# Kernel tuning notes

Measured on AMD Instinct MI355X. Metric: run time of the kernel, lower is better.

Reference implementation:

```python
import jax, jax.numpy as jnp
import numpy as np

S, B, E, H = 2048, 32, 1024, 1024

def setup_inputs() -> dict:
    key = jax.random.key(0)
    k1, k2, k3, k4, k5 = jax.random.split(key, 5)
    h_t = jax.random.normal(k1, (1, B, H), dtype=jnp.float32)
    h_enc = jax.random.normal(k2, (S, B, E), dtype=jnp.float32)
    # nn.Linear weights stored as (out, in); scaled like default init
    W_enc = jax.random.normal(k3, (H, E), dtype=jnp.float32) / np.sqrt(E)
    W_dec = jax.random.normal(k4, (H, H), dtype=jnp.float32) / np.sqrt(H)
    w_score = jax.random.normal(k5, (1, H), dtype=jnp.float32) / np.sqrt(H)
    return {"h_t": h_t, "h_enc": h_enc, "W_enc": W_enc, "W_dec": W_dec, "w_score": w_score}

def reference(h_t, h_enc, W_enc, W_dec, w_score):
    # h_enc: (S,B,E) -> (B,S,E); h_t: (1,B,H) -> (B,1,H)
    he = jnp.transpose(h_enc, (1, 0, 2))
    ht = jnp.transpose(h_t, (1, 0, 2))
    compr_he = jnp.einsum('bse,he->bsh', he, W_enc)          # (B,S,H)
    compr_ht = jnp.einsum('bth,gh->btg', ht, W_dec)          # (B,1,H), broadcasts over S
    # Linear(H,1) -> Tanh -> Softmax over seq dim
    scores = jnp.tanh(jnp.einsum('bsh,oh->bso', compr_he + compr_ht, w_score))  # (B,S,1)
    alphas = jax.nn.softmax(scores, axis=1)                  # (B,S,1)
    context = jnp.sum(he * alphas, axis=1)[None]             # (1,B,E)
    return (context, alphas)
```

## Files before the change

### kernel.cpp

```cpp
#include <hip/hip_runtime.h>
#include <hip/hip_bf16.h>

#define S_DIM 2048
#define B_DIM 32
#define E_DIM 1024
#define H_DIM 1024

#define VCHUNKS 32

#define CH 8
#define WPB 4
#define ROWS_PER_BLOCK (CH * WPB)
#define BLOCKS_PER_B (S_DIM / ROWS_PER_BLOCK)
#define NBLK (B_DIM * BLOCKS_PER_B)


__global__ __launch_bounds__(256) void k1_partial_v(
    const float* __restrict__ W_enc, const float* __restrict__ W_dec,
    const float* __restrict__ w_score, float* __restrict__ penc,
    float* __restrict__ pdec) {
  int bid = blockIdx.x;
  int t = threadIdx.x;
  bool enc = bid < 128;
  int idx = enc ? bid : bid - 128;
  int hc = idx >> 2;
  int e0 = (idx & 3) << 8;
  const float* M = enc ? W_enc : W_dec;
  int h0 = hc * 32;
  float acc = 0.f;
#pragma unroll 8
  for (int r = 0; r < 32; ++r) {
    float w = w_score[h0 + r];
    acc = fmaf(w, M[(size_t)(h0 + r) * E_DIM + e0 + t], acc);
  }
  float* dst = enc ? penc : pdec;
  dst[hc * E_DIM + e0 + t] = acc;
}

__global__ __launch_bounds__(256) void k2_finalize_v(
    const float* __restrict__ penc, const float* __restrict__ pdec,
    float* __restrict__ venc, float* __restrict__ vdec) {
  int g = blockIdx.x * 256 + threadIdx.x;
  bool enc = g < E_DIM;
  const float* p = enc ? penc : pdec;
  int e = enc ? g : g - E_DIM;
  float acc = 0.f;
#pragma unroll 8
  for (int c = 0; c < VCHUNKS; ++c) acc += p[c * E_DIM + e];
  (enc ? venc : vdec)[e] = acc;
}

__device__ __forceinline__ float wave_allreduce_sum(float v) {
#pragma unroll
  for (int off = 1; off < 64; off <<= 1) v += __shfl_xor(v, off, 64);
  return v;
}

__device__ __forceinline__ float fast_tanh(float x) {
  float e2 = __expf(2.f * x);
  return 1.f - 2.f * __builtin_amdgcn_rcpf(e2 + 1.f);
}

__global__ __launch_bounds__(256) void k3_stream(
    const float* __restrict__ h_enc, const float* __restrict__ h_t,
    const float* __restrict__ venc, const float* __restrict__ vdec,
    float* __restrict__ expw, float* __restrict__ pl,
    float* __restrict__ pctx) {
  int bid = blockIdx.x;
  int t = threadIdx.x;
  int w = t >> 6;
  int lane = t & 63;
  int b = bid >> 6;
  int cbi = bid & 63;
  int s0 = cbi * ROWS_PER_BLOCK + w * CH;
  int e_base = lane * 4;

  __shared__ float lctx[WPB][E_DIM];
  __shared__ float ll[WPB];

  float4 ve[4];
#pragma unroll
  for (int k = 0; k < 4; ++k)
    ve[k] = *reinterpret_cast<const float4*>(venc + e_base + k * 256);

  float cb = 0.f;
#pragma unroll
  for (int k = 0; k < 4; ++k) {
    float4 vd = *reinterpret_cast<const float4*>(vdec + e_base + k * 256);
    float4 ht = *reinterpret_cast<const float4*>(h_t + b * H_DIM + e_base + k * 256);
    cb = fmaf(vd.x, ht.x, cb);
    cb = fmaf(vd.y, ht.y, cb);
    cb = fmaf(vd.z, ht.z, cb);
    cb = fmaf(vd.w, ht.w, cb);
  }
  cb = wave_allreduce_sum(cb);

  float4 ctx[4];
#pragma unroll
  for (int k = 0; k < 4; ++k) ctx[k] = make_float4(0.f, 0.f, 0.f, 0.f);
  float lsum = 0.f;

  for (int s = s0; s < s0 + CH; ++s) {
    const float* row = h_enc + ((size_t)s * B_DIM + b) * E_DIM + e_base;
    float4 a[4];
#pragma unroll
    for (int k = 0; k < 4; ++k)
      a[k] = *reinterpret_cast<const float4*>(row + k * 256);

    float d = 0.f;
#pragma unroll
    for (int k = 0; k < 4; ++k) {
      d = fmaf(a[k].x, ve[k].x, d);
      d = fmaf(a[k].y, ve[k].y, d);
      d = fmaf(a[k].z, ve[k].z, d);
      d = fmaf(a[k].w, ve[k].w, d);
    }
    d = wave_allreduce_sum(d);

    float wgt = __expf(fast_tanh(d + cb));
    if (lane == 0) expw[b * S_DIM + s] = wgt;
    lsum += wgt;

#pragma unroll
    for (int k = 0; k < 4; ++k) {
      ctx[k].x = fmaf(wgt, a[k].x, ctx[k].x);
      ctx[k].y = fmaf(wgt, a[k].y, ctx[k].y);
      ctx[k].z = fmaf(wgt, a[k].z, ctx[k].z);
      ctx[k].w = fmaf(wgt, a[k].w, ctx[k].w);
    }
  }

#pragma unroll
  for (int k = 0; k < 4; ++k)
    *reinterpret_cast<float4*>(&lctx[w][e_base + k * 256]) = ctx[k];
  if (lane == 0) ll[w] = lsum;
  __syncthreads();

  {
    int e = t * 4;
    float4 v0 = *reinterpret_cast<const float4*>(&lctx[0][e]);
    float4 v1 = *reinterpret_cast<const float4*>(&lctx[1][e]);
    float4 v2 = *reinterpret_cast<const float4*>(&lctx[2][e]);
    float4 v3 = *reinterpret_cast<const float4*>(&lctx[3][e]);
    float4 r;
    r.x = (v0.x + v1.x) + (v2.x + v3.x);
    r.y = (v0.y + v1.y) + (v2.y + v3.y);
    r.z = (v0.z + v1.z) + (v2.z + v3.z);
    r.w = (v0.w + v1.w) + (v2.w + v3.w);
    *reinterpret_cast<float4*>(pctx + (size_t)bid * E_DIM + e) = r;
    if (t == 0) pl[bid] = (ll[0] + ll[1]) + (ll[2] + ll[3]);
  }
}

__global__ __launch_bounds__(256) void k4_finalize(
    const float* __restrict__ pl, const float* __restrict__ pctx,
    const float* __restrict__ expw, float* __restrict__ out) {
  int bid = blockIdx.x;
  int t = threadIdx.x;
  int lane = t & 63;
  bool isCtx = bid < 256;
  int idx = isCtx ? bid : bid - 256;
  int b = idx >> 3;

  __shared__ float s_l;
  __shared__ float s_half[128];

  if (t < 64) {
    float v = pl[b * BLOCKS_PER_B + lane];
    v = wave_allreduce_sum(v);
    if (lane == 0) s_l = v;
  }
  __syncthreads();
  float lb = s_l;

  if (isCtx) {
    int e0 = (idx & 7) * 128;
    int eo = t & 127;
    int c0 = (t >> 7) * 32;
    const float* base = pctx + (size_t)(b * BLOCKS_PER_B + c0) * E_DIM + e0 + eo;
    float acc = 0.f;
#pragma unroll 8
    for (int c = 0; c < 32; ++c) acc += base[(size_t)c * E_DIM];
    if (t >= 128) s_half[eo] = acc;
    __syncthreads();
    if (t < 128) out[b * E_DIM + e0 + eo] = (acc + s_half[eo]) / lb;
  } else {
    int sb = (idx & 7) * 256;
    int o = b * S_DIM + sb + t;
    out[B_DIM * E_DIM + o] = expw[o] / lb;
  }
}

extern "C" void kernel_launch(void* const* d_in, const int* in_sizes, int n_in,
                              void* d_out, int out_size, void* d_ws, size_t ws_size,
                              hipStream_t stream) {
  const float* h_t     = (const float*)d_in[0];
  const float* h_enc   = (const float*)d_in[1];
  const float* W_enc   = (const float*)d_in[2];
  const float* W_dec   = (const float*)d_in[3];
  const float* w_score = (const float*)d_in[4];
  float* out = (float*)d_out;
  float* ws = (float*)d_ws;

  float* penc = ws;
  float* pdec = penc + 32768;
  float* venc = pdec + 32768;
  float* vdec = venc + 1024;
  float* expw = vdec + 1024;
  float* pl   = expw + 65536;
  float* pctx = pl + 2048;

  hipLaunchKernelGGL(k1_partial_v, dim3(256), dim3(256), 0, stream,
                     W_enc, W_dec, w_score, penc, pdec);
  hipLaunchKernelGGL(k2_finalize_v, dim3(8), dim3(256), 0, stream,
                     penc, pdec, venc, vdec);
  hipLaunchKernelGGL(k3_stream, dim3(NBLK), dim3(256), 0, stream,
                     h_enc, h_t, venc, vdec, expw, pl, pctx);
  hipLaunchKernelGGL(k4_finalize, dim3(512), dim3(256), 0, stream,
                     pl, pctx, expw, out);
}
```

Before: 58.78 us.

## Remap stream kernel so each wave handles one batch over 32 contiguous rows

```diff
diff --git a/kernel.cpp b/kernel.cpp
--- a/kernel.cpp
+++ b/kernel.cpp
@@ -8,11 +8,12 @@
 
 #define VCHUNKS 32
 
-#define CH 8
-#define WPB 4
-#define ROWS_PER_BLOCK (CH * WPB)
-#define BLOCKS_PER_B (S_DIM / ROWS_PER_BLOCK)
-#define NBLK (B_DIM * BLOCKS_PER_B)
+#define CH 32
+#define BPG 4
+#define NBG (B_DIM / BPG)
+#define SCH (S_DIM / CH)
+#define NBLK (NBG * SCH)
+#define PARTS_PER_B SCH
 
 
 __global__ __launch_bounds__(256) void k1_partial_v(
@@ -70,13 +71,11 @@
   int t = threadIdx.x;
   int w = t >> 6;
   int lane = t & 63;
-  int b = bid >> 6;
-  int cbi = bid & 63;
-  int s0 = cbi * ROWS_PER_BLOCK + w * CH;
+  int bg = bid & (NBG - 1);
+  int si = bid >> 3;
+  int b = bg * BPG + w;
+  int s0 = si * CH;
   int e_base = lane * 4;
-
-  __shared__ float lctx[WPB][E_DIM];
-  __shared__ float ll[WPB];
 
   float4 ve[4];
 #pragma unroll
@@ -130,26 +129,12 @@
     }
   }
 
+  int prow = si * B_DIM + b;
+  float* pc = pctx + (size_t)prow * E_DIM + e_base;
 #pragma unroll
   for (int k = 0; k < 4; ++k)
-    *reinterpret_cast<float4*>(&lctx[w][e_base + k * 256]) = ctx[k];
-  if (lane == 0) ll[w] = lsum;
-  __syncthreads();
-
-  {
-    int e = t * 4;
-    float4 v0 = *reinterpret_cast<const float4*>(&lctx[0][e]);
-    float4 v1 = *reinterpret_cast<const float4*>(&lctx[1][e]);
-    float4 v2 = *reinterpret_cast<const float4*>(&lctx[2][e]);
-    float4 v3 = *reinterpret_cast<const float4*>(&lctx[3][e]);
-    float4 r;
-    r.x = (v0.x + v1.x) + (v2.x + v3.x);
-    r.y = (v0.y + v1.y) + (v2.y + v3.y);
-    r.z = (v0.z + v1.z) + (v2.z + v3.z);
-    r.w = (v0.w + v1.w) + (v2.w + v3.w);
-    *reinterpret_cast<float4*>(pctx + (size_t)bid * E_DIM + e) = r;
-    if (t == 0) pl[bid] = (ll[0] + ll[1]) + (ll[2] + ll[3]);
-  }
+    *reinterpret_cast<float4*>(pc + k * 256) = ctx[k];
+  if (lane == 0) pl[prow] = lsum;
 }
 
 __global__ __launch_bounds__(256) void k4_finalize(
@@ -157,7 +142,6 @@
     const float* __restrict__ expw, float* __restrict__ out) {
   int bid = blockIdx.x;
   int t = threadIdx.x;
-  int lane = t & 63;
   bool isCtx = bid < 256;
   int idx = isCtx ? bid : bid - 256;
   int b = idx >> 3;
@@ -166,9 +150,9 @@
   __shared__ float s_half[128];
 
   if (t < 64) {
-    float v = pl[b * BLOCKS_PER_B + lane];
+    float v = pl[t * B_DIM + b];
     v = wave_allreduce_sum(v);
-    if (lane == 0) s_l = v;
+    if (t == 0) s_l = v;
   }
   __syncthreads();
   float lb = s_l;
@@ -177,10 +161,12 @@
     int e0 = (idx & 7) * 128;
     int eo = t & 127;
     int c0 = (t >> 7) * 32;
-    const float* base = pctx + (size_t)(b * BLOCKS_PER_B + c0) * E_DIM + e0 + eo;
     float acc = 0.f;
 #pragma unroll 8
-    for (int c = 0; c < 32; ++c) acc += base[(size_t)c * E_DIM];
+    for (int j = 0; j < 32; ++j) {
+      int row = (c0 + j) * B_DIM + b;
+      acc += pctx[(size_t)row * E_DIM + e0 + eo];
+    }
     if (t >= 128) s_half[eo] = acc;
     __syncthreads();
     if (t < 128) out[b * E_DIM + e0 + eo] = (acc + s_half[eo]) / lb;
```

Result: faster. 57.10 us (-2.9%).
